# Optimization experiments

Measured on AMD Instinct MI355X. Metric: run time of the kernel, lower is better.

## Reference

```python
import jax, jax.numpy as jnp
import numpy as np

UNITS = 256  # intr_dim


def _lstm_scan(x, W, U, b):
    """Keras-style LSTM (gate order i,f,c,o), return last hidden state.
    x: [B,T,D], W: [D,4H], U: [H,4H], b: [4H] -> h_last [B,H]"""
    B = x.shape[0]
    H = U.shape[0]
    # precompute input projections for all timesteps: [T,B,4H]
    xw = jnp.einsum('btd,dg->tbg', x, W) + b

    def step(carry, xw_t):
        h, c = carry
        z = xw_t + h @ U  # [B,4H]
        i = jax.nn.sigmoid(z[:, :H])
        f = jax.nn.sigmoid(z[:, H:2 * H])
        g = jnp.tanh(z[:, 2 * H:3 * H])
        o = jax.nn.sigmoid(z[:, 3 * H:])
        c_new = f * c + i * g
        h_new = o * jnp.tanh(c_new)
        return (h_new, c_new), None

    init = (jnp.zeros((B, H), x.dtype), jnp.zeros((B, H), x.dtype))
    (h_last, _), _ = jax.lax.scan(step, init, xw)
    return h_last


def setup_inputs() -> dict:
    key = jax.random.key(0)
    ks = jax.random.split(key, 6)
    B, T, D, H = 64, 2048, 256, UNITS
    s = 1.0 / np.sqrt(D)
    sr = 1.0 / np.sqrt(H)
    return {
        'x': jax.random.normal(ks[0], (B, T, D), jnp.float32),
        'Wf': jax.random.normal(ks[1], (D, 4 * H), jnp.float32) * s,
        'Uf': jax.random.normal(ks[2], (H, 4 * H), jnp.float32) * sr,
        'bf': jnp.zeros((4 * H,), jnp.float32),
        'Wb': jax.random.normal(ks[3], (D, 4 * H), jnp.float32) * s,
        'Ub': jax.random.normal(ks[4], (H, 4 * H), jnp.float32) * sr,
        'bb': jnp.zeros((4 * H,), jnp.float32),
    }


def reference(x, Wf, Uf, bf, Wb, Ub, bb):
    # Bidirectional LSTM, return_sequences=False, merge_mode='concat'.
    # Recurrent dropout and output Dropout are identity at inference.
    h_fwd = _lstm_scan(x, Wf, Uf, bf)
    h_bwd = _lstm_scan(x[:, ::-1, :], Wb, Ub, bb)
    return jnp.concatenate([h_fwd, h_bwd], axis=-1)  # [B, 2H]
```

## Files before the change

### kernel.cpp

```cpp
#include <hip/hip_runtime.h>

#define T_TOTAL 2048

typedef short bf16x8 __attribute__((ext_vector_type(8)));
typedef float f32x4 __attribute__((ext_vector_type(4)));
typedef unsigned long long ull;

#define OFF_WT  0ull
#define OFF_UT  (1ull<<20)
#define OFF_EX  (2ull<<20)
#define OFF_HFR (OFF_EX + (256ull<<10))
#define OFF_CST (OFF_HFR + (64ull<<10))
#define OFF_XW  (3ull<<20)
#define STEP_BYTES 262144ull

__device__ __forceinline__ unsigned short f2bf(float f){
  unsigned int u = __builtin_bit_cast(unsigned int, f);
  u += 0x7fffu + ((u>>16)&1u);
  return (unsigned short)(u>>16);
}
__device__ __forceinline__ float bfhi2f(unsigned int u){
  unsigned int v = u & 0xffff0000u; return __builtin_bit_cast(float, v);
}
__device__ __forceinline__ float bflo2f(unsigned int u){
  unsigned int v = u << 16; return __builtin_bit_cast(float, v);
}
__device__ __forceinline__ float sigf(float z){ return 1.0f/(1.0f + __expf(-z)); }
__device__ __forceinline__ float tanhf_(float z){ return 2.0f/(1.0f + __expf(-2.0f*z)) - 1.0f; }

__global__ __launch_bounds__(256) void kprep(const float* __restrict__ Wf, const float* __restrict__ Uf,
                                             const float* __restrict__ Wb, const float* __restrict__ Ub,
                                             unsigned short* __restrict__ ws){
  __shared__ float tile[64][65];
  int mat = blockIdx.z;
  const float* src = (mat==0)?Wf:(mat==1)?Wb:(mat==2)?Uf:Ub;
  unsigned short* dst = ws + ((mat<2)?0u:524288u) + (unsigned)(mat&1)*262144u;
  int c0 = blockIdx.x*64, k0 = blockIdx.y*64;
  int tx = threadIdx.x & 63, ty = threadIdx.x >> 6;
  #pragma unroll
  for (int j=0;j<16;j++){
    int r = j*4+ty;
    tile[r][tx] = src[(size_t)(k0+r)*1024 + (c0+tx)];
  }
  __syncthreads();
  #pragma unroll
  for (int j=0;j<16;j++){
    int r = j*4+ty;
    int col = c0+r, k = k0+tx;
    int cg = col>>4, ks = k>>5, kq = (k>>3)&3, e = k&7;
    dst[(size_t)(cg*8+ks)*512 + ((col&15)+16*kq)*8 + e] = f2bf(tile[tx][r]);
  }
}

__global__ __launch_bounds__(512) void kgemm(const float* __restrict__ x,
        const float* __restrict__ biasF, const float* __restrict__ biasB,
        const unsigned short* __restrict__ wsu, char* __restrict__ xw,
        int s0, int Tthis){
  __shared__ __align__(16) char smem[147456];
  char* abuf = smem + 131072;
  int chunk = blockIdx.x, dir = blockIdx.y, q = blockIdx.z;
  int tid = threadIdx.x, w = tid>>6, l = tid&63;
  int l15 = l&15;
  const char* WT = (const char*)(wsu + (size_t)dir*262144u);
  const float* bias = dir ? biasB : biasF;

  bf16x8 wfrA[8][4];
  bf16x8 wfrV[8][2];
  #pragma unroll
  for (int ct=0;ct<8;ct++){
    int cg = 8*w + ct;
    const char* base = WT + (size_t)cg*8192 + (size_t)l*16;
    #pragma unroll
    for (int ks=0;ks<4;ks++) wfrA[ct][ks] = *(const bf16x8*)(base + ks*1024);
    wfrV[ct][0] = *(const bf16x8*)(base + 4*1024);
    wfrV[ct][1] = *(const bf16x8*)(base + 5*1024);
    #pragma unroll
    for (int k2=0;k2<2;k2++){
      bf16x8 t = *(const bf16x8*)(base + (6+k2)*1024);
      *(bf16x8*)(smem + ((cg*2+k2)*1024 + l*16)) = t;
    }
  }
  float bv[8];
  #pragma unroll
  for (int ct=0;ct<8;ct++) bv[ct] = bias[128*w + ct*16 + l15];

  int b_loc = tid>>5, kk = (tid&31)*8;
  int b = q*16 + b_loc;
  int aslot = (kk>>5)*1024 + (b_loc + 16*((kk>>3)&3))*16;

  int nt = Tthis - chunk*64; if (nt > 64) nt = 64; if (nt < 0) nt = 0;
  if (nt > 0){
    int sg = s0 + chunk*64;
    int t_src = dir ? (T_TOTAL-1-sg) : sg;
    const float* px = x + ((size_t)b*T_TOTAL + t_src)*256 + kk;
    float4 v0 = *(const float4*)px;
    float4 v1 = *(const float4*)(px+4);
    uint4 pk;
    pk.x = (unsigned)f2bf(v0.x) | ((unsigned)f2bf(v0.y)<<16);
    pk.y = (unsigned)f2bf(v0.z) | ((unsigned)f2bf(v0.w)<<16);
    pk.z = (unsigned)f2bf(v1.x) | ((unsigned)f2bf(v1.y)<<16);
    pk.w = (unsigned)f2bf(v1.z) | ((unsigned)f2bf(v1.w)<<16);
    *(uint4*)(abuf + aslot) = pk;
  }
  __syncthreads();

  int p = 0;
  for (int tl=0; tl<nt; ++tl){
    float4 v0, v1;
    int have_next = (tl+1 < nt);
    if (have_next){
      int sg = s0 + chunk*64 + tl + 1;
      int t_src = dir ? (T_TOTAL-1-sg) : sg;
      const float* px = x + ((size_t)b*T_TOTAL + t_src)*256 + kk;
      v0 = *(const float4*)px;
      v1 = *(const float4*)(px+4);
    }
    char* outp = xw + (size_t)(chunk*64+tl)*STEP_BYTES + (size_t)dir*131072u + (size_t)q*32768u;
    #pragma unroll
    for (int half=0; half<2; ++half){
      f32x4 acc[4];
      #pragma unroll
      for (int ci=0;ci<4;ci++){
        float b0 = bv[half*4+ci];
        acc[ci][0]=b0; acc[ci][1]=b0; acc[ci][2]=b0; acc[ci][3]=b0;
      }
      #pragma unroll
      for (int ks=0;ks<4;ks++){
        bf16x8 a = *(const bf16x8*)(abuf + p*8192 + ks*1024 + l*16);
        #pragma unroll
        for (int ci=0;ci<4;ci++)
          acc[ci] = __builtin_amdgcn_mfma_f32_16x16x32_bf16(a, wfrA[half*4+ci][ks], acc[ci], 0, 0, 0);
      }
      #pragma unroll
      for (int k2=0;k2<2;k2++){
        bf16x8 a = *(const bf16x8*)(abuf + p*8192 + (4+k2)*1024 + l*16);
        #pragma unroll
        for (int ci=0;ci<4;ci++)
          acc[ci] = __builtin_amdgcn_mfma_f32_16x16x32_bf16(a, wfrV[half*4+ci][k2], acc[ci], 0, 0, 0);
      }
      #pragma unroll
      for (int k2=0;k2<2;k2++){
        bf16x8 a = *(const bf16x8*)(abuf + p*8192 + (6+k2)*1024 + l*16);
        #pragma unroll
        for (int ci=0;ci<4;ci++){
          bf16x8 bb = *(const bf16x8*)(smem + (((8*w+half*4+ci)*2+k2)*1024 + l*16));
          acc[ci] = __builtin_amdgcn_mfma_f32_16x16x32_bf16(a, bb, acc[ci], 0, 0, 0);
        }
      }
      #pragma unroll
      for (int ci=0;ci<4;ci++){
        int col = 128*w + (half*4+ci)*16 + l15;
        uint2 pk;
        pk.x = (unsigned)f2bf(acc[ci][0]) | ((unsigned)f2bf(acc[ci][1])<<16);
        pk.y = (unsigned)f2bf(acc[ci][2]) | ((unsigned)f2bf(acc[ci][3])<<16);
        *(uint2*)(outp + (size_t)col*32 + (l>>4)*8) = pk;
      }
    }
    if (have_next){
      uint4 pk;
      pk.x = (unsigned)f2bf(v0.x) | ((unsigned)f2bf(v0.y)<<16);
      pk.y = (unsigned)f2bf(v0.z) | ((unsigned)f2bf(v0.w)<<16);
      pk.z = (unsigned)f2bf(v1.x) | ((unsigned)f2bf(v1.y)<<16);
      pk.w = (unsigned)f2bf(v1.z) | ((unsigned)f2bf(v1.w)<<16);
      *(uint4*)(abuf + (p^1)*8192 + aslot) = pk;
    }
    __syncthreads();
    p ^= 1;
  }
}

__global__ __launch_bounds__(512) void krec(const unsigned short* __restrict__ wsu,
        const char* __restrict__ xw, char* __restrict__ ex, char* __restrict__ hfr,
        float* __restrict__ cst, float* __restrict__ out,
        int nsteps, int s0, int last){
  __shared__ __align__(16) char Bl[131072];
  __shared__ __align__(16) char Ab[16384];
  int bid = blockIdx.x;
  int hs = bid>>3, dir = (bid>>2)&1, bq = bid&3;
  int tid = threadIdx.x, w = tid>>6, l = tid&63;
  int l15 = l&15;
  const char* UT = (const char*)(wsu + 524288u + (size_t)dir*262144u);

  bf16x8 Bf[2][8];
  #pragma unroll
  for (int g=0; g<2; g++){
    int cg = g*16 + hs*8 + w;
    const char* base = UT + (size_t)cg*8192 + (size_t)l*16;
    #pragma unroll
    for (int k2=0;k2<4;k2++){
      Bf[g][k2]   = *(const bf16x8*)(base + (size_t)(4*hs+k2)*1024);
      Bf[g][4+k2] = *(const bf16x8*)(base + (size_t)(4*(1-hs)+k2)*1024);
    }
  }
  #pragma unroll
  for (int g=2; g<4; g++){
    int cg = g*16 + hs*8 + w;
    #pragma unroll
    for (int ks=0;ks<8;ks++){
      bf16x8 t = *(const bf16x8*)(UT + (size_t)(cg*8+ks)*1024 + (size_t)l*16);
      *(bf16x8*)(Bl + ((w*2+(g-2))*8+ks)*1024 + l*16) = t;
    }
  }

  int grp = dir*4 + bq;
  char* exbase = ex + (size_t)grp*32768u;

  int jh = w*16 + l15;
  int ksl = jh>>5, kqh = (jh>>3)&3, eh = jh&7;
  int jfull = hs*128 + jh;
  int bg = l>>4;
  int offr0 = ksl*1024 + (bg*4 + 0 + 16*kqh)*16 + eh*2;
  int offr1 = ksl*1024 + (bg*4 + 1 + 16*kqh)*16 + eh*2;
  int offr2 = ksl*1024 + (bg*4 + 2 + 16*kqh)*16 + eh*2;
  int offr3 = ksl*1024 + (bg*4 + 3 + 16*kqh)*16 + eh*2;

  float c_[4];
  if (s0 == 0){
    #pragma unroll
    for (int r=0;r<4;r++) c_[r] = 0.0f;
    *(uint4*)(Ab + tid*16) = make_uint4(0u,0u,0u,0u);
  } else {
    *(uint4*)(Ab + tid*16) = *(const uint4*)(hfr + (size_t)grp*8192u + tid*16);
    #pragma unroll
    for (int r=0;r<4;r++)
      c_[r] = cst[((size_t)dir*64 + bq*16 + bg*4 + r)*256 + jfull];
  }
  __syncthreads();

  const char* XW = xw + (size_t)dir*131072u + (size_t)bq*32768u;
  uint2 xv[4];
  #pragma unroll
  for (int g=0;g<4;g++){
    int col = g*256 + hs*128 + w*16 + l15;
    xv[g] = *(const uint2*)(XW + (size_t)col*32 + bg*8);
  }

  const char* Bl0 = Bl + (w*2+0)*8192 + l*16;
  const char* Bl1 = Bl + (w*2+1)*8192 + l*16;
  int ownkoff = hs*4096, partkoff = (1-hs)*4096;

  for (int lt=0; lt<nsteps; ++lt){
    int par = lt&1, parn = par^1;
    unsigned short wantu = (unsigned short)(unsigned)(s0 + lt);
    f32x4 acc[4];
    #pragma unroll
    for (int g=0;g<4;g++){
      uint2 v = xv[g];
      acc[g][0]=bflo2f(v.x); acc[g][1]=bfhi2f(v.x);
      acc[g][2]=bflo2f(v.y); acc[g][3]=bfhi2f(v.y);
    }
    {
      const char* Aown = Ab + par*8192 + ownkoff + l*16;
      #pragma unroll
      for (int k2=0;k2<4;k2++){
        bf16x8 a = *(const bf16x8*)(Aown + k2*1024);
        acc[0] = __builtin_amdgcn_mfma_f32_16x16x32_bf16(a, Bf[0][k2], acc[0], 0, 0, 0);
        acc[1] = __builtin_amdgcn_mfma_f32_16x16x32_bf16(a, Bf[1][k2], acc[1], 0, 0, 0);
        bf16x8 b2 = *(const bf16x8*)(Bl0 + ownkoff + k2*1024);
        acc[2] = __builtin_amdgcn_mfma_f32_16x16x32_bf16(a, b2, acc[2], 0, 0, 0);
        bf16x8 b3 = *(const bf16x8*)(Bl1 + ownkoff + k2*1024);
        acc[3] = __builtin_amdgcn_mfma_f32_16x16x32_bf16(a, b3, acc[3], 0, 0, 0);
      }
    }
    if (lt > 0){
      const ull* exr = (const ull*)(exbase + (size_t)par*16384u + (size_t)(1-hs)*8192u) + 2*tid;
      ull v0, v1;
      for(;;){
        v0 = __hip_atomic_load(exr, __ATOMIC_RELAXED, __HIP_MEMORY_SCOPE_AGENT);
        if ((unsigned short)(v0>>48) == wantu) break;
        __builtin_amdgcn_s_sleep(1);
      }
      for(;;){
        v1 = __hip_atomic_load(exr+1, __ATOMIC_RELAXED, __HIP_MEMORY_SCOPE_AGENT);
        if ((unsigned short)(v1>>48) == wantu) break;
        __builtin_amdgcn_s_sleep(1);
      }
      char* ap = Ab + par*8192 + partkoff;
      *(unsigned short*)(ap + offr0) = (unsigned short)v0;
      *(unsigned short*)(ap + offr1) = (unsigned short)(v0>>16);
      *(unsigned short*)(ap + offr2) = (unsigned short)v1;
      *(unsigned short*)(ap + offr3) = (unsigned short)(v1>>16);
    }
    __syncthreads();
    {
      const char* Apart = Ab + par*8192 + partkoff + l*16;
      #pragma unroll
      for (int k2=0;k2<4;k2++){
        bf16x8 a = *(const bf16x8*)(Apart + k2*1024);
        acc[0] = __builtin_amdgcn_mfma_f32_16x16x32_bf16(a, Bf[0][4+k2], acc[0], 0, 0, 0);
        acc[1] = __builtin_amdgcn_mfma_f32_16x16x32_bf16(a, Bf[1][4+k2], acc[1], 0, 0, 0);
        bf16x8 b2 = *(const bf16x8*)(Bl0 + partkoff + k2*1024);
        acc[2] = __builtin_amdgcn_mfma_f32_16x16x32_bf16(a, b2, acc[2], 0, 0, 0);
        bf16x8 b3 = *(const bf16x8*)(Bl1 + partkoff + k2*1024);
        acc[3] = __builtin_amdgcn_mfma_f32_16x16x32_bf16(a, b3, acc[3], 0, 0, 0);
      }
    }
    float hv[4];
    #pragma unroll
    for (int r=0;r<4;r++){
      float ig = sigf(acc[0][r]);
      float fg = sigf(acc[1][r]);
      float gg = tanhf_(acc[2][r]);
      float og = sigf(acc[3][r]);
      float cn = fg*c_[r] + ig*gg;
      c_[r] = cn;
      hv[r] = og*tanhf_(cn);
    }

    if (lt == nsteps-1){
      if (last){
        #pragma unroll
        for (int r=0;r<4;r++)
          out[(size_t)(bq*16 + bg*4 + r)*512 + dir*256 + jfull] = hv[r];
      } else {
        char* hw = hfr + (size_t)grp*8192u + hs*4096;
        *(unsigned short*)(hw + offr0) = f2bf(hv[0]);
        *(unsigned short*)(hw + offr1) = f2bf(hv[1]);
        *(unsigned short*)(hw + offr2) = f2bf(hv[2]);
        *(unsigned short*)(hw + offr3) = f2bf(hv[3]);
        #pragma unroll
        for (int r=0;r<4;r++)
          cst[((size_t)dir*64 + bq*16 + bg*4 + r)*256 + jfull] = c_[r];
      }
      break;
    }

    unsigned short hb0 = f2bf(hv[0]), hb1 = f2bf(hv[1]);
    unsigned short hb2 = f2bf(hv[2]), hb3 = f2bf(hv[3]);
    {
      ull tag = ((ull)(unsigned short)(unsigned)(s0+lt+1)) << 48;
      ull p0 = (ull)hb0 | ((ull)hb1<<16) | tag;
      ull p1 = (ull)hb2 | ((ull)hb3<<16) | tag;
      ull* exw = (ull*)(exbase + (size_t)parn*16384u + (size_t)hs*8192u) + 2*tid;
      __hip_atomic_store(exw,   p0, __ATOMIC_RELAXED, __HIP_MEMORY_SCOPE_AGENT);
      __hip_atomic_store(exw+1, p1, __ATOMIC_RELAXED, __HIP_MEMORY_SCOPE_AGENT);
    }
    {
      char* al = Ab + parn*8192 + ownkoff;
      *(unsigned short*)(al + offr0) = hb0;
      *(unsigned short*)(al + offr1) = hb1;
      *(unsigned short*)(al + offr2) = hb2;
      *(unsigned short*)(al + offr3) = hb3;
    }
    #pragma unroll
    for (int g=0;g<4;g++){
      int col = g*256 + hs*128 + w*16 + l15;
      xv[g] = *(const uint2*)(XW + (size_t)(lt+1)*STEP_BYTES + (size_t)col*32 + bg*8);
    }
    __syncthreads();
  }
}

extern "C" void kernel_launch(void* const* d_in, const int* in_sizes, int n_in,
                              void* d_out, int out_size, void* d_ws, size_t ws_size,
                              hipStream_t stream){
  (void)in_sizes; (void)n_in; (void)out_size;
  const float* x   = (const float*)d_in[0];
  const float* Wf  = (const float*)d_in[1];
  const float* Uf  = (const float*)d_in[2];
  const float* bf_ = (const float*)d_in[3];
  const float* Wb  = (const float*)d_in[4];
  const float* Ub  = (const float*)d_in[5];
  const float* bb  = (const float*)d_in[6];
  float* out = (float*)d_out;
  char* ws = (char*)d_ws;
  unsigned short* wsu = (unsigned short*)ws;
  char* ex  = ws + OFF_EX;
  char* hfr = ws + OFF_HFR;
  float* cst = (float*)(ws + OFF_CST);
  char* xwb = ws + OFF_XW;

  (void)hipMemsetAsync(ex, 0, 262144, stream);
  kprep<<<dim3(16,4,4), 256, 0, stream>>>(Wf, Uf, Wb, Ub, wsu);

  long long avail = (long long)ws_size - (long long)OFF_XW;
  int Tseg = (avail > 0) ? (int)(avail / (long long)STEP_BYTES) : 1;
  if (Tseg < 1) Tseg = 1;
  if (Tseg > T_TOTAL) Tseg = T_TOTAL;
  int nseg = (T_TOTAL + Tseg - 1)/Tseg;
  int s0 = 0;
  for (int seg=0; seg<nseg; ++seg){
    int Tthis = (T_TOTAL - s0 < Tseg) ? (T_TOTAL - s0) : Tseg;
    int nchunk = (Tthis + 63)/64;
    kgemm<<<dim3(nchunk,2,4), 512, 0, stream>>>(x, bf_, bb, wsu, xwb, s0, Tthis);
    krec<<<dim3(16), 512, 0, stream>>>(wsu, xwb, ex, hfr, cst, out, Tthis, s0,
                                       (seg==nseg-1)?1:0);
    s0 += Tthis;
  }
}
```

Measured before the change: 6.117 ms.

## Interleave two batch quarters per recurrent block to hide cross-block exchange latency

Each recurrent block now processes two batch quarters in alternation, and the grid halves from 16 to 8 blocks. While one quarter waits on the partner block's hidden-state exchange, the other quarter's MFMA and gate work can proceed, which is meant to hide the exchange latency. The s_sleep in the spin-wait loops is also removed to cut polling latency. The cost is double per-block serial work and twice as many __syncthreads per timestep, so the step loop may get longer if latency was not the bottleneck.

```diff
diff --git a/kernel.cpp b/kernel.cpp
--- a/kernel.cpp
+++ b/kernel.cpp
@@ -174,9 +174,9 @@
         float* __restrict__ cst, float* __restrict__ out,
         int nsteps, int s0, int last){
   __shared__ __align__(16) char Bl[131072];
-  __shared__ __align__(16) char Ab[16384];
+  __shared__ __align__(16) char Ab[32768];
   int bid = blockIdx.x;
-  int hs = bid>>3, dir = (bid>>2)&1, bq = bid&3;
+  int hs = bid>>2, dir = (bid>>1)&1, bp = bid&1;
   int tid = threadIdx.x, w = tid>>6, l = tid&63;
   int l15 = l&15;
   const char* UT = (const char*)(wsu + 524288u + (size_t)dir*262144u);
@@ -201,9 +201,6 @@
       *(bf16x8*)(Bl + ((w*2+(g-2))*8+ks)*1024 + l*16) = t;
     }
   }
-
-  int grp = dir*4 + bq;
-  char* exbase = ex + (size_t)grp*32768u;
 
   int jh = w*16 + l15;
   int ksl = jh>>5, kqh = (jh>>3)&3, eh = jh&7;
@@ -214,26 +211,29 @@
   int offr2 = ksl*1024 + (bg*4 + 2 + 16*kqh)*16 + eh*2;
   int offr3 = ksl*1024 + (bg*4 + 3 + 16*kqh)*16 + eh*2;
 
-  float c_[4];
-  if (s0 == 0){
-    #pragma unroll
-    for (int r=0;r<4;r++) c_[r] = 0.0f;
-    *(uint4*)(Ab + tid*16) = make_uint4(0u,0u,0u,0u);
-  } else {
-    *(uint4*)(Ab + tid*16) = *(const uint4*)(hfr + (size_t)grp*8192u + tid*16);
-    #pragma unroll
-    for (int r=0;r<4;r++)
-      c_[r] = cst[((size_t)dir*64 + bq*16 + bg*4 + r)*256 + jfull];
+  float c_[2][4];
+  uint2 xv[2][4];
+  #pragma unroll
+  for (int c=0;c<2;c++){
+    int bq = 2*bp + c, grp = dir*4 + bq;
+    if (s0 == 0){
+      #pragma unroll
+      for (int r=0;r<4;r++) c_[c][r] = 0.0f;
+      *(uint4*)(Ab + c*16384 + tid*16) = make_uint4(0u,0u,0u,0u);
+    } else {
+      *(uint4*)(Ab + c*16384 + tid*16) = *(const uint4*)(hfr + (size_t)grp*8192u + tid*16);
+      #pragma unroll
+      for (int r=0;r<4;r++)
+        c_[c][r] = cst[((size_t)dir*64 + bq*16 + bg*4 + r)*256 + jfull];
+    }
+    const char* XWc = xw + (size_t)dir*131072u + (size_t)bq*32768u;
+    #pragma unroll
+    for (int g=0;g<4;g++){
+      int col = g*256 + hs*128 + w*16 + l15;
+      xv[c][g] = *(const uint2*)(XWc + (size_t)col*32 + bg*8);
+    }
   }
   __syncthreads();
-
-  const char* XW = xw + (size_t)dir*131072u + (size_t)bq*32768u;
-  uint2 xv[4];
-  #pragma unroll
-  for (int g=0;g<4;g++){
-    int col = g*256 + hs*128 + w*16 + l15;
-    xv[g] = *(const uint2*)(XW + (size_t)col*32 + bg*8);
-  }
 
   const char* Bl0 = Bl + (w*2+0)*8192 + l*16;
   const char* Bl1 = Bl + (w*2+1)*8192 + l*16;
@@ -242,112 +242,117 @@
   for (int lt=0; lt<nsteps; ++lt){
     int par = lt&1, parn = par^1;
     unsigned short wantu = (unsigned short)(unsigned)(s0 + lt);
-    f32x4 acc[4];
-    #pragma unroll
-    for (int g=0;g<4;g++){
-      uint2 v = xv[g];
-      acc[g][0]=bflo2f(v.x); acc[g][1]=bfhi2f(v.x);
-      acc[g][2]=bflo2f(v.y); acc[g][3]=bfhi2f(v.y);
-    }
-    {
-      const char* Aown = Ab + par*8192 + ownkoff + l*16;
-      #pragma unroll
-      for (int k2=0;k2<4;k2++){
-        bf16x8 a = *(const bf16x8*)(Aown + k2*1024);
-        acc[0] = __builtin_amdgcn_mfma_f32_16x16x32_bf16(a, Bf[0][k2], acc[0], 0, 0, 0);
-        acc[1] = __builtin_amdgcn_mfma_f32_16x16x32_bf16(a, Bf[1][k2], acc[1], 0, 0, 0);
-        bf16x8 b2 = *(const bf16x8*)(Bl0 + ownkoff + k2*1024);
-        acc[2] = __builtin_amdgcn_mfma_f32_16x16x32_bf16(a, b2, acc[2], 0, 0, 0);
-        bf16x8 b3 = *(const bf16x8*)(Bl1 + ownkoff + k2*1024);
-        acc[3] = __builtin_amdgcn_mfma_f32_16x16x32_bf16(a, b3, acc[3], 0, 0, 0);
-      }
-    }
-    if (lt > 0){
-      const ull* exr = (const ull*)(exbase + (size_t)par*16384u + (size_t)(1-hs)*8192u) + 2*tid;
-      ull v0, v1;
-      for(;;){
-        v0 = __hip_atomic_load(exr, __ATOMIC_RELAXED, __HIP_MEMORY_SCOPE_AGENT);
-        if ((unsigned short)(v0>>48) == wantu) break;
-        __builtin_amdgcn_s_sleep(1);
-      }
-      for(;;){
-        v1 = __hip_atomic_load(exr+1, __ATOMIC_RELAXED, __HIP_MEMORY_SCOPE_AGENT);
-        if ((unsigned short)(v1>>48) == wantu) break;
-        __builtin_amdgcn_s_sleep(1);
-      }
-      char* ap = Ab + par*8192 + partkoff;
-      *(unsigned short*)(ap + offr0) = (unsigned short)v0;
-      *(unsigned short*)(ap + offr1) = (unsigned short)(v0>>16);
-      *(unsigned short*)(ap + offr2) = (unsigned short)v1;
-      *(unsigned short*)(ap + offr3) = (unsigned short)(v1>>16);
-    }
-    __syncthreads();
-    {
-      const char* Apart = Ab + par*8192 + partkoff + l*16;
-      #pragma unroll
-      for (int k2=0;k2<4;k2++){
-        bf16x8 a = *(const bf16x8*)(Apart + k2*1024);
-        acc[0] = __builtin_amdgcn_mfma_f32_16x16x32_bf16(a, Bf[0][4+k2], acc[0], 0, 0, 0);
-        acc[1] = __builtin_amdgcn_mfma_f32_16x16x32_bf16(a, Bf[1][4+k2], acc[1], 0, 0, 0);
-        bf16x8 b2 = *(const bf16x8*)(Bl0 + partkoff + k2*1024);
-        acc[2] = __builtin_amdgcn_mfma_f32_16x16x32_bf16(a, b2, acc[2], 0, 0, 0);
-        bf16x8 b3 = *(const bf16x8*)(Bl1 + partkoff + k2*1024);
-        acc[3] = __builtin_amdgcn_mfma_f32_16x16x32_bf16(a, b3, acc[3], 0, 0, 0);
-      }
-    }
-    float hv[4];
-    #pragma unroll
-    for (int r=0;r<4;r++){
-      float ig = sigf(acc[0][r]);
-      float fg = sigf(acc[1][r]);
-      float gg = tanhf_(acc[2][r]);
-      float og = sigf(acc[3][r]);
-      float cn = fg*c_[r] + ig*gg;
-      c_[r] = cn;
-      hv[r] = og*tanhf_(cn);
-    }
-
-    if (lt == nsteps-1){
-      if (last){
-        #pragma unroll
-        for (int r=0;r<4;r++)
-          out[(size_t)(bq*16 + bg*4 + r)*512 + dir*256 + jfull] = hv[r];
+    #pragma unroll
+    for (int c=0;c<2;c++){
+      int bq = 2*bp + c, grp = dir*4 + bq;
+      char* exbase = ex + (size_t)grp*32768u;
+      const char* XWc = xw + (size_t)dir*131072u + (size_t)bq*32768u;
+      char* Abc = Ab + c*16384;
+
+      f32x4 acc[4];
+      #pragma unroll
+      for (int g=0;g<4;g++){
+        uint2 v = xv[c][g];
+        acc[g][0]=bflo2f(v.x); acc[g][1]=bfhi2f(v.x);
+        acc[g][2]=bflo2f(v.y); acc[g][3]=bfhi2f(v.y);
+      }
+      {
+        const char* Aown = Abc + par*8192 + ownkoff + l*16;
+        #pragma unroll
+        for (int k2=0;k2<4;k2++){
+          bf16x8 a = *(const bf16x8*)(Aown + k2*1024);
+          acc[0] = __builtin_amdgcn_mfma_f32_16x16x32_bf16(a, Bf[0][k2], acc[0], 0, 0, 0);
+          acc[1] = __builtin_amdgcn_mfma_f32_16x16x32_bf16(a, Bf[1][k2], acc[1], 0, 0, 0);
+          bf16x8 b2 = *(const bf16x8*)(Bl0 + ownkoff + k2*1024);
+          acc[2] = __builtin_amdgcn_mfma_f32_16x16x32_bf16(a, b2, acc[2], 0, 0, 0);
+          bf16x8 b3 = *(const bf16x8*)(Bl1 + ownkoff + k2*1024);
+          acc[3] = __builtin_amdgcn_mfma_f32_16x16x32_bf16(a, b3, acc[3], 0, 0, 0);
+        }
+      }
+      if (lt > 0){
+        const ull* exr = (const ull*)(exbase + (size_t)par*16384u + (size_t)(1-hs)*8192u) + 2*tid;
+        ull v0, v1;
+        for(;;){
+          v0 = __hip_atomic_load(exr, __ATOMIC_RELAXED, __HIP_MEMORY_SCOPE_AGENT);
+          if ((unsigned short)(v0>>48) == wantu) break;
+        }
+        for(;;){
+          v1 = __hip_atomic_load(exr+1, __ATOMIC_RELAXED, __HIP_MEMORY_SCOPE_AGENT);
+          if ((unsigned short)(v1>>48) == wantu) break;
+        }
+        char* ap = Abc + par*8192 + partkoff;
+        *(unsigned short*)(ap + offr0) = (unsigned short)v0;
+        *(unsigned short*)(ap + offr1) = (unsigned short)(v0>>16);
+        *(unsigned short*)(ap + offr2) = (unsigned short)v1;
+        *(unsigned short*)(ap + offr3) = (unsigned short)(v1>>16);
+      }
+      __syncthreads();
+      {
+        const char* Apart = Abc + par*8192 + partkoff + l*16;
+        #pragma unroll
+        for (int k2=0;k2<4;k2++){
+          bf16x8 a = *(const bf16x8*)(Apart + k2*1024);
+          acc[0] = __builtin_amdgcn_mfma_f32_16x16x32_bf16(a, Bf[0][4+k2], acc[0], 0, 0, 0);
+          acc[1] = __builtin_amdgcn_mfma_f32_16x16x32_bf16(a, Bf[1][4+k2], acc[1], 0, 0, 0);
+          bf16x8 b2 = *(const bf16x8*)(Bl0 + partkoff + k2*1024);
+          acc[2] = __builtin_amdgcn_mfma_f32_16x16x32_bf16(a, b2, acc[2], 0, 0, 0);
+          bf16x8 b3 = *(const bf16x8*)(Bl1 + partkoff + k2*1024);
+          acc[3] = __builtin_amdgcn_mfma_f32_16x16x32_bf16(a, b3, acc[3], 0, 0, 0);
+        }
+      }
+      float hv[4];
+      #pragma unroll
+      for (int r=0;r<4;r++){
+        float ig = sigf(acc[0][r]);
+        float fg = sigf(acc[1][r]);
+        float gg = tanhf_(acc[2][r]);
+        float og = sigf(acc[3][r]);
+        float cn = fg*c_[c][r] + ig*gg;
+        c_[c][r] = cn;
+        hv[r] = og*tanhf_(cn);
+      }
+
+      if (lt == nsteps-1){
+        if (last){
+          #pragma unroll
+          for (int r=0;r<4;r++)
+            out[(size_t)(bq*16 + bg*4 + r)*512 + dir*256 + jfull] = hv[r];
+        } else {
+          char* hw = hfr + (size_t)grp*8192u + hs*4096;
+          *(unsigned short*)(hw + offr0) = f2bf(hv[0]);
+          *(unsigned short*)(hw + offr1) = f2bf(hv[1]);
+          *(unsigned short*)(hw + offr2) = f2bf(hv[2]);
+          *(unsigned short*)(hw + offr3) = f2bf(hv[3]);
+          #pragma unroll
+          for (int r=0;r<4;r++)
+            cst[((size_t)dir*64 + bq*16 + bg*4 + r)*256 + jfull] = c_[c][r];
+        }
       } else {
-        char* hw = hfr + (size_t)grp*8192u + hs*4096;
-        *(unsigned short*)(hw + offr0) = f2bf(hv[0]);
-        *(unsigned short*)(hw + offr1) = f2bf(hv[1]);
-        *(unsigned short*)(hw + offr2) = f2bf(hv[2]);
-        *(unsigned short*)(hw + offr3) = f2bf(hv[3]);
-        #pragma unroll
-        for (int r=0;r<4;r++)
-          cst[((size_t)dir*64 + bq*16 + bg*4 + r)*256 + jfull] = c_[r];
-      }
-      break;
-    }
-
-    unsigned short hb0 = f2bf(hv[0]), hb1 = f2bf(hv[1]);
-    unsigned short hb2 = f2bf(hv[2]), hb3 = f2bf(hv[3]);
-    {
-      ull tag = ((ull)(unsigned short)(unsigned)(s0+lt+1)) << 48;
-      ull p0 = (ull)hb0 | ((ull)hb1<<16) | tag;
-      ull p1 = (ull)hb2 | ((ull)hb3<<16) | tag;
-      ull* exw = (ull*)(exbase + (size_t)parn*16384u + (size_t)hs*8192u) + 2*tid;
-      __hip_atomic_store(exw,   p0, __ATOMIC_RELAXED, __HIP_MEMORY_SCOPE_AGENT);
-      __hip_atomic_store(exw+1, p1, __ATOMIC_RELAXED, __HIP_MEMORY_SCOPE_AGENT);
-    }
-    {
-      char* al = Ab + parn*8192 + ownkoff;
-      *(unsigned short*)(al + offr0) = hb0;
-      *(unsigned short*)(al + offr1) = hb1;
-      *(unsigned short*)(al + offr2) = hb2;
-      *(unsigned short*)(al + offr3) = hb3;
-    }
-    #pragma unroll
-    for (int g=0;g<4;g++){
-      int col = g*256 + hs*128 + w*16 + l15;
-      xv[g] = *(const uint2*)(XW + (size_t)(lt+1)*STEP_BYTES + (size_t)col*32 + bg*8);
-    }
-    __syncthreads();
+        unsigned short hb0 = f2bf(hv[0]), hb1 = f2bf(hv[1]);
+        unsigned short hb2 = f2bf(hv[2]), hb3 = f2bf(hv[3]);
+        {
+          ull tag = ((ull)(unsigned short)(unsigned)(s0+lt+1)) << 48;
+          ull p0 = (ull)hb0 | ((ull)hb1<<16) | tag;
+          ull p1 = (ull)hb2 | ((ull)hb3<<16) | tag;
+          ull* exw = (ull*)(exbase + (size_t)parn*16384u + (size_t)hs*8192u) + 2*tid;
+          __hip_atomic_store(exw,   p0, __ATOMIC_RELAXED, __HIP_MEMORY_SCOPE_AGENT);
+          __hip_atomic_store(exw+1, p1, __ATOMIC_RELAXED, __HIP_MEMORY_SCOPE_AGENT);
+        }
+        {
+          char* al = Abc + parn*8192 + ownkoff;
+          *(unsigned short*)(al + offr0) = hb0;
+          *(unsigned short*)(al + offr1) = hb1;
+          *(unsigned short*)(al + offr2) = hb2;
+          *(unsigned short*)(al + offr3) = hb3;
+        }
+        #pragma unroll
+        for (int g=0;g<4;g++){
+          int col = g*256 + hs*128 + w*16 + l15;
+          xv[c][g] = *(const uint2*)(XWc + (size_t)(lt+1)*STEP_BYTES + (size_t)col*32 + bg*8);
+        }
+      }
+      __syncthreads();
+    }
   }
 }
 
@@ -383,8 +388,8 @@
     int Tthis = (T_TOTAL - s0 < Tseg) ? (T_TOTAL - s0) : Tseg;
     int nchunk = (Tthis + 63)/64;
     kgemm<<<dim3(nchunk,2,4), 512, 0, stream>>>(x, bf_, bb, wsu, xwb, s0, Tthis);
-    krec<<<dim3(16), 512, 0, stream>>>(wsu, xwb, ex, hfr, cst, out, Tthis, s0,
-                                       (seg==nseg-1)?1:0);
+    krec<<<dim3(8), 512, 0, stream>>>(wsu, xwb, ex, hfr, cst, out, Tthis, s0,
+                                      (seg==nseg-1)?1:0);
     s0 += Tthis;
   }
 }
```

New measurement: 11.54 ms. 88.6% more time.

## Fuse input-projection GEMM and recurrence into one kernel with per-chunk ready flags

Applied to the files above, without the earlier changes.

Merges the separate input-projection GEMM kernel and the recurrent kernel into a single launch. The first 16 blocks run the recurrence, and the remaining blocks compute the input projection in chunks of 16 timesteps, each setting a flag when its chunk is written. The recurrent blocks spin on the flag for the next chunk, so the projection work overlaps the serial recurrence instead of finishing completely before it starts. The risks are deadlock if the recurrent blocks are not co-resident with the producer blocks, extra global flag traffic and polling, and a small reorder of the exchange polling loop.

```diff
diff --git a/kernel.cpp b/kernel.cpp
--- a/kernel.cpp
+++ b/kernel.cpp
@@ -1,6 +1,7 @@
 #include <hip/hip_runtime.h>
 
 #define T_TOTAL 2048
+#define CH 16
 
 typedef short bf16x8 __attribute__((ext_vector_type(8)));
 typedef float f32x4 __attribute__((ext_vector_type(4)));
@@ -9,8 +10,9 @@
 #define OFF_WT  0ull
 #define OFF_UT  (1ull<<20)
 #define OFF_EX  (2ull<<20)
-#define OFF_HFR (OFF_EX + (256ull<<10))
-#define OFF_CST (OFF_HFR + (64ull<<10))
+#define OFF_FLG (OFF_EX + (256ull<<10))
+#define OFF_HFR (OFF_EX + (320ull<<10))
+#define OFF_CST (OFF_EX + (384ull<<10))
 #define OFF_XW  (3ull<<20)
 #define STEP_BYTES 262144ull
 
@@ -52,133 +54,139 @@
   }
 }
 
-__global__ __launch_bounds__(512) void kgemm(const float* __restrict__ x,
+__global__ __launch_bounds__(512) void kfused(const float* __restrict__ x,
         const float* __restrict__ biasF, const float* __restrict__ biasB,
         const unsigned short* __restrict__ wsu, char* __restrict__ xw,
-        int s0, int Tthis){
-  __shared__ __align__(16) char smem[147456];
-  char* abuf = smem + 131072;
-  int chunk = blockIdx.x, dir = blockIdx.y, q = blockIdx.z;
+        char* __restrict__ ex, unsigned int* __restrict__ flg,
+        char* __restrict__ hfr, float* __restrict__ cst, float* __restrict__ out,
+        int nsteps, int s0, int last){
+  __shared__ __align__(16) char Bl[131072];
+  __shared__ __align__(16) char Ab[16384];
   int tid = threadIdx.x, w = tid>>6, l = tid&63;
   int l15 = l&15;
-  const char* WT = (const char*)(wsu + (size_t)dir*262144u);
-  const float* bias = dir ? biasB : biasF;
-
-  bf16x8 wfrA[8][4];
-  bf16x8 wfrV[8][2];
-  #pragma unroll
-  for (int ct=0;ct<8;ct++){
-    int cg = 8*w + ct;
-    const char* base = WT + (size_t)cg*8192 + (size_t)l*16;
-    #pragma unroll
-    for (int ks=0;ks<4;ks++) wfrA[ct][ks] = *(const bf16x8*)(base + ks*1024);
-    wfrV[ct][0] = *(const bf16x8*)(base + 4*1024);
-    wfrV[ct][1] = *(const bf16x8*)(base + 5*1024);
-    #pragma unroll
-    for (int k2=0;k2<2;k2++){
-      bf16x8 t = *(const bf16x8*)(base + (6+k2)*1024);
-      *(bf16x8*)(smem + ((cg*2+k2)*1024 + l*16)) = t;
-    }
-  }
-  float bv[8];
-  #pragma unroll
-  for (int ct=0;ct<8;ct++) bv[ct] = bias[128*w + ct*16 + l15];
-
-  int b_loc = tid>>5, kk = (tid&31)*8;
-  int b = q*16 + b_loc;
-  int aslot = (kk>>5)*1024 + (b_loc + 16*((kk>>3)&3))*16;
-
-  int nt = Tthis - chunk*64; if (nt > 64) nt = 64; if (nt < 0) nt = 0;
-  if (nt > 0){
-    int sg = s0 + chunk*64;
-    int t_src = dir ? (T_TOTAL-1-sg) : sg;
-    const float* px = x + ((size_t)b*T_TOTAL + t_src)*256 + kk;
-    float4 v0 = *(const float4*)px;
-    float4 v1 = *(const float4*)(px+4);
-    uint4 pk;
-    pk.x = (unsigned)f2bf(v0.x) | ((unsigned)f2bf(v0.y)<<16);
-    pk.y = (unsigned)f2bf(v0.z) | ((unsigned)f2bf(v0.w)<<16);
-    pk.z = (unsigned)f2bf(v1.x) | ((unsigned)f2bf(v1.y)<<16);
-    pk.w = (unsigned)f2bf(v1.z) | ((unsigned)f2bf(v1.w)<<16);
-    *(uint4*)(abuf + aslot) = pk;
-  }
-  __syncthreads();
-
-  int p = 0;
-  for (int tl=0; tl<nt; ++tl){
-    float4 v0, v1;
-    int have_next = (tl+1 < nt);
-    if (have_next){
-      int sg = s0 + chunk*64 + tl + 1;
+
+  if (blockIdx.x >= 16){
+    int gb = blockIdx.x - 16;
+    int chunk = gb>>3, dir = (gb>>2)&1, q = gb&3;
+    char* abuf = Ab;
+    const char* WT = (const char*)(wsu + (size_t)dir*262144u);
+    const float* bias = dir ? biasB : biasF;
+
+    bf16x8 wfrA[8][4];
+    bf16x8 wfrV[8][2];
+    #pragma unroll
+    for (int ct=0;ct<8;ct++){
+      int cg = 8*w + ct;
+      const char* base = WT + (size_t)cg*8192 + (size_t)l*16;
+      #pragma unroll
+      for (int ks=0;ks<4;ks++) wfrA[ct][ks] = *(const bf16x8*)(base + ks*1024);
+      wfrV[ct][0] = *(const bf16x8*)(base + 4*1024);
+      wfrV[ct][1] = *(const bf16x8*)(base + 5*1024);
+      #pragma unroll
+      for (int k2=0;k2<2;k2++){
+        bf16x8 t = *(const bf16x8*)(base + (6+k2)*1024);
+        *(bf16x8*)(Bl + ((cg*2+k2)*1024 + l*16)) = t;
+      }
+    }
+    float bv[8];
+    #pragma unroll
+    for (int ct=0;ct<8;ct++) bv[ct] = bias[128*w + ct*16 + l15];
+
+    int b_loc = tid>>5, kk = (tid&31)*8;
+    int b = q*16 + b_loc;
+    int aslot = (kk>>5)*1024 + (b_loc + 16*((kk>>3)&3))*16;
+
+    int nt = nsteps - chunk*CH; if (nt > CH) nt = CH; if (nt < 0) nt = 0;
+    if (nt > 0){
+      int sg = s0 + chunk*CH;
       int t_src = dir ? (T_TOTAL-1-sg) : sg;
       const float* px = x + ((size_t)b*T_TOTAL + t_src)*256 + kk;
-      v0 = *(const float4*)px;
-      v1 = *(const float4*)(px+4);
-    }
-    char* outp = xw + (size_t)(chunk*64+tl)*STEP_BYTES + (size_t)dir*131072u + (size_t)q*32768u;
-    #pragma unroll
-    for (int half=0; half<2; ++half){
-      f32x4 acc[4];
-      #pragma unroll
-      for (int ci=0;ci<4;ci++){
-        float b0 = bv[half*4+ci];
-        acc[ci][0]=b0; acc[ci][1]=b0; acc[ci][2]=b0; acc[ci][3]=b0;
-      }
-      #pragma unroll
-      for (int ks=0;ks<4;ks++){
-        bf16x8 a = *(const bf16x8*)(abuf + p*8192 + ks*1024 + l*16);
-        #pragma unroll
-        for (int ci=0;ci<4;ci++)
-          acc[ci] = __builtin_amdgcn_mfma_f32_16x16x32_bf16(a, wfrA[half*4+ci][ks], acc[ci], 0, 0, 0);
-      }
-      #pragma unroll
-      for (int k2=0;k2<2;k2++){
-        bf16x8 a = *(const bf16x8*)(abuf + p*8192 + (4+k2)*1024 + l*16);
-        #pragma unroll
-        for (int ci=0;ci<4;ci++)
-          acc[ci] = __builtin_amdgcn_mfma_f32_16x16x32_bf16(a, wfrV[half*4+ci][k2], acc[ci], 0, 0, 0);
-      }
-      #pragma unroll
-      for (int k2=0;k2<2;k2++){
-        bf16x8 a = *(const bf16x8*)(abuf + p*8192 + (6+k2)*1024 + l*16);
-        #pragma unroll
-        for (int ci=0;ci<4;ci++){
-          bf16x8 bb = *(const bf16x8*)(smem + (((8*w+half*4+ci)*2+k2)*1024 + l*16));
-          acc[ci] = __builtin_amdgcn_mfma_f32_16x16x32_bf16(a, bb, acc[ci], 0, 0, 0);
-        }
-      }
-      #pragma unroll
-      for (int ci=0;ci<4;ci++){
-        int col = 128*w + (half*4+ci)*16 + l15;
-        uint2 pk;
-        pk.x = (unsigned)f2bf(acc[ci][0]) | ((unsigned)f2bf(acc[ci][1])<<16);
-        pk.y = (unsigned)f2bf(acc[ci][2]) | ((unsigned)f2bf(acc[ci][3])<<16);
-        *(uint2*)(outp + (size_t)col*32 + (l>>4)*8) = pk;
-      }
-    }
-    if (have_next){
+      float4 v0 = *(const float4*)px;
+      float4 v1 = *(const float4*)(px+4);
       uint4 pk;
       pk.x = (unsigned)f2bf(v0.x) | ((unsigned)f2bf(v0.y)<<16);
       pk.y = (unsigned)f2bf(v0.z) | ((unsigned)f2bf(v0.w)<<16);
       pk.z = (unsigned)f2bf(v1.x) | ((unsigned)f2bf(v1.y)<<16);
       pk.w = (unsigned)f2bf(v1.z) | ((unsigned)f2bf(v1.w)<<16);
-      *(uint4*)(abuf + (p^1)*8192 + aslot) = pk;
+      *(uint4*)(abuf + aslot) = pk;
     }
     __syncthreads();
-    p ^= 1;
-  }
-}
-
-__global__ __launch_bounds__(512) void krec(const unsigned short* __restrict__ wsu,
-        const char* __restrict__ xw, char* __restrict__ ex, char* __restrict__ hfr,
-        float* __restrict__ cst, float* __restrict__ out,
-        int nsteps, int s0, int last){
-  __shared__ __align__(16) char Bl[131072];
-  __shared__ __align__(16) char Ab[16384];
+
+    int p = 0;
+    for (int tl=0; tl<nt; ++tl){
+      float4 v0, v1;
+      int have_next = (tl+1 < nt);
+      if (have_next){
+        int sg = s0 + chunk*CH + tl + 1;
+        int t_src = dir ? (T_TOTAL-1-sg) : sg;
+        const float* px = x + ((size_t)b*T_TOTAL + t_src)*256 + kk;
+        v0 = *(const float4*)px;
+        v1 = *(const float4*)(px+4);
+      }
+      char* outp = xw + (size_t)(chunk*CH+tl)*STEP_BYTES + (size_t)dir*131072u + (size_t)q*32768u;
+      #pragma unroll
+      for (int half=0; half<2; ++half){
+        f32x4 acc[4];
+        #pragma unroll
+        for (int ci=0;ci<4;ci++){
+          float b0 = bv[half*4+ci];
+          acc[ci][0]=b0; acc[ci][1]=b0; acc[ci][2]=b0; acc[ci][3]=b0;
+        }
+        #pragma unroll
+        for (int ks=0;ks<4;ks++){
+          bf16x8 a = *(const bf16x8*)(abuf + p*8192 + ks*1024 + l*16);
+          #pragma unroll
+          for (int ci=0;ci<4;ci++)
+            acc[ci] = __builtin_amdgcn_mfma_f32_16x16x32_bf16(a, wfrA[half*4+ci][ks], acc[ci], 0, 0, 0);
+        }
+        #pragma unroll
+        for (int k2=0;k2<2;k2++){
+          bf16x8 a = *(const bf16x8*)(abuf + p*8192 + (4+k2)*1024 + l*16);
+          #pragma unroll
+          for (int ci=0;ci<4;ci++)
+            acc[ci] = __builtin_amdgcn_mfma_f32_16x16x32_bf16(a, wfrV[half*4+ci][k2], acc[ci], 0, 0, 0);
+        }
+        #pragma unroll
+        for (int k2=0;k2<2;k2++){
+          bf16x8 a = *(const bf16x8*)(abuf + p*8192 + (6+k2)*1024 + l*16);
+          #pragma unroll
+          for (int ci=0;ci<4;ci++){
+            bf16x8 bb = *(const bf16x8*)(Bl + (((8*w+half*4+ci)*2+k2)*1024 + l*16));
+            acc[ci] = __builtin_amdgcn_mfma_f32_16x16x32_bf16(a, bb, acc[ci], 0, 0, 0);
+          }
+        }
+        #pragma unroll
+        for (int ci=0;ci<4;ci++){
+          int col = 128*w + (half*4+ci)*16 + l15;
+          uint2 pk;
+          pk.x = (unsigned)f2bf(acc[ci][0]) | ((unsigned)f2bf(acc[ci][1])<<16);
+          pk.y = (unsigned)f2bf(acc[ci][2]) | ((unsigned)f2bf(acc[ci][3])<<16);
+          __hip_atomic_store((ull*)(outp + (size_t)col*32 + (l>>4)*8),
+                             __builtin_bit_cast(ull, pk),
+                             __ATOMIC_RELAXED, __HIP_MEMORY_SCOPE_AGENT);
+        }
+      }
+      if (have_next){
+        uint4 pk;
+        pk.x = (unsigned)f2bf(v0.x) | ((unsigned)f2bf(v0.y)<<16);
+        pk.y = (unsigned)f2bf(v0.z) | ((unsigned)f2bf(v0.w)<<16);
+        pk.z = (unsigned)f2bf(v1.x) | ((unsigned)f2bf(v1.y)<<16);
+        pk.w = (unsigned)f2bf(v1.z) | ((unsigned)f2bf(v1.w)<<16);
+        *(uint4*)(abuf + (p^1)*8192 + aslot) = pk;
+      }
+      __syncthreads();
+      p ^= 1;
+    }
+    asm volatile("s_waitcnt vmcnt(0)" ::: "memory");
+    __syncthreads();
+    if (tid == 0 && nt > 0)
+      __hip_atomic_store(&flg[((size_t)chunk*8 + dir*4 + q)*16], 1u,
+                         __ATOMIC_RELAXED, __HIP_MEMORY_SCOPE_AGENT);
+    return;
+  }
+
   int bid = blockIdx.x;
   int hs = bid>>3, dir = (bid>>2)&1, bq = bid&3;
-  int tid = threadIdx.x, w = tid>>6, l = tid&63;
-  int l15 = l&15;
   const char* UT = (const char*)(wsu + 524288u + (size_t)dir*262144u);
 
   bf16x8 Bf[2][8];
@@ -202,7 +210,7 @@
     }
   }
 
-  int grp = dir*4 + bq;
+  int grp = dir*4 + bq, dq = dir*4 + bq;
   char* exbase = ex + (size_t)grp*32768u;
 
   int jh = w*16 + l15;
@@ -227,6 +235,9 @@
   }
   __syncthreads();
 
+  while (__hip_atomic_load(&flg[(size_t)0*8*16 + dq*16], __ATOMIC_RELAXED, __HIP_MEMORY_SCOPE_AGENT) == 0u)
+    __builtin_amdgcn_s_sleep(8);
+
   const char* XW = xw + (size_t)dir*131072u + (size_t)bq*32768u;
   uint2 xv[4];
   #pragma unroll
@@ -264,16 +275,15 @@
     }
     if (lt > 0){
       const ull* exr = (const ull*)(exbase + (size_t)par*16384u + (size_t)(1-hs)*8192u) + 2*tid;
-      ull v0, v1;
-      for(;;){
+      ull v0 = __hip_atomic_load(exr,   __ATOMIC_RELAXED, __HIP_MEMORY_SCOPE_AGENT);
+      ull v1 = __hip_atomic_load(exr+1, __ATOMIC_RELAXED, __HIP_MEMORY_SCOPE_AGENT);
+      while ((unsigned short)(v0>>48) != wantu){
+        __builtin_amdgcn_s_sleep(1);
         v0 = __hip_atomic_load(exr, __ATOMIC_RELAXED, __HIP_MEMORY_SCOPE_AGENT);
-        if ((unsigned short)(v0>>48) == wantu) break;
+      }
+      while ((unsigned short)(v1>>48) != wantu){
         __builtin_amdgcn_s_sleep(1);
-      }
-      for(;;){
         v1 = __hip_atomic_load(exr+1, __ATOMIC_RELAXED, __HIP_MEMORY_SCOPE_AGENT);
-        if ((unsigned short)(v1>>48) == wantu) break;
-        __builtin_amdgcn_s_sleep(1);
       }
       char* ap = Ab + par*8192 + partkoff;
       *(unsigned short*)(ap + offr0) = (unsigned short)v0;
@@ -342,10 +352,18 @@
       *(unsigned short*)(al + offr2) = hb2;
       *(unsigned short*)(al + offr3) = hb3;
     }
-    #pragma unroll
-    for (int g=0;g<4;g++){
-      int col = g*256 + hs*128 + w*16 + l15;
-      xv[g] = *(const uint2*)(XW + (size_t)(lt+1)*STEP_BYTES + (size_t)col*32 + bg*8);
+    {
+      int ltn = lt+1;
+      if ((ltn & (CH-1)) == 0){
+        int ck = ltn >> 4;
+        while (__hip_atomic_load(&flg[((size_t)ck*8 + dq)*16], __ATOMIC_RELAXED, __HIP_MEMORY_SCOPE_AGENT) == 0u)
+          __builtin_amdgcn_s_sleep(8);
+      }
+      #pragma unroll
+      for (int g=0;g<4;g++){
+        int col = g*256 + hs*128 + w*16 + l15;
+        xv[g] = *(const uint2*)(XW + (size_t)ltn*STEP_BYTES + (size_t)col*32 + bg*8);
+      }
     }
     __syncthreads();
   }
@@ -366,6 +384,7 @@
   char* ws = (char*)d_ws;
   unsigned short* wsu = (unsigned short*)ws;
   char* ex  = ws + OFF_EX;
+  unsigned int* flg = (unsigned int*)(ws + OFF_FLG);
   char* hfr = ws + OFF_HFR;
   float* cst = (float*)(ws + OFF_CST);
   char* xwb = ws + OFF_XW;
@@ -381,10 +400,11 @@
   int s0 = 0;
   for (int seg=0; seg<nseg; ++seg){
     int Tthis = (T_TOTAL - s0 < Tseg) ? (T_TOTAL - s0) : Tseg;
-    int nchunk = (Tthis + 63)/64;
-    kgemm<<<dim3(nchunk,2,4), 512, 0, stream>>>(x, bf_, bb, wsu, xwb, s0, Tthis);
-    krec<<<dim3(16), 512, 0, stream>>>(wsu, xwb, ex, hfr, cst, out, Tthis, s0,
-                                       (seg==nseg-1)?1:0);
+    int nchunk = (Tthis + CH - 1)/CH;
+    (void)hipMemsetAsync(flg, 0, 65536, stream);
+    kfused<<<dim3(16 + 8*nchunk), 512, 0, stream>>>(x, bf_, bb, wsu, xwb,
+                                                    ex, flg, hfr, cst, out,
+                                                    Tthis, s0, (seg==nseg-1)?1:0);
     s0 += Tthis;
   }
 }
```

After: 5.837 ms. 1.05x faster.
